# Performance work log

Measured on AMD Instinct MI355X. Metric: run time of the kernel, lower is better.

The kernel has to match this reference:

```python
import jax, jax.numpy as jnp
import numpy as np

N, D, H, E, OUT, TOP_K = 16384, 1024, 4096, 8, 4096, 2


def setup_inputs() -> dict:
    key = jax.random.key(0)
    ks = jax.random.split(key, 9)
    s_d = 1.0 / np.sqrt(D)
    s_h = 1.0 / np.sqrt(H)
    return {
        "x": jax.random.normal(ks[0], (N, D), dtype=jnp.float32),
        "W_in": jax.random.normal(ks[1], (D, D), dtype=jnp.float32) * s_d,
        "b_in": jax.random.normal(ks[2], (D,), dtype=jnp.float32) * 0.01,
        "W_gate": jax.random.normal(ks[3], (D, E), dtype=jnp.float32) * s_d,
        "W1": jax.random.normal(ks[4], (E, D, H), dtype=jnp.float32) * s_d,
        "b1": jax.random.normal(ks[5], (E, H), dtype=jnp.float32) * 0.01,
        "W2": jax.random.normal(ks[6], (E, H, D), dtype=jnp.float32) * s_h,
        "b2": jax.random.normal(ks[7], (E, D), dtype=jnp.float32) * 0.01,
        "W_head": jax.random.normal(ks[8], (D, OUT), dtype=jnp.float32) * s_d,
    }


def reference(x, W_in, b_in, W_gate, W1, b1, W2, b2, W_head):
    # Input linear: [N, D]
    h = x @ W_in + b_in

    # Gating: softmax over experts, keep top-k, renormalize
    probs = jax.nn.softmax(h @ W_gate, axis=-1)            # [N, E]
    top_vals, top_idx = jax.lax.top_k(probs, TOP_K)        # [N, K]
    top_vals = top_vals / jnp.sum(top_vals, axis=-1, keepdims=True)
    rows = jnp.arange(h.shape[0])[:, None]
    combine = jnp.zeros_like(probs).at[rows, top_idx].set(top_vals)  # [N, E]

    # Expert FFNs, weighted combine (loop over small fixed expert count)
    moe_out = jnp.zeros_like(h)
    for e in range(E):
        he = jax.nn.relu(h @ W1[e] + b1[e])                # [N, H]
        ye = he @ W2[e] + b2[e]                            # [N, D]
        moe_out = moe_out + combine[:, e:e + 1] * ye

    # Head (no bias)
    return moe_out @ W_head
```

## Files before the change

kernel.cpp:

```cpp
#include <hip/hip_runtime.h>
#include <math.h>

#define NN 16384
#define DD 1024
#define HH 4096
#define EE 8
#define OUTD 4096

typedef unsigned short u16;
typedef short v8s __attribute__((ext_vector_type(8)));
typedef float v4f __attribute__((ext_vector_type(4)));

__device__ __forceinline__ u16 f2bf(float f) {
    unsigned int u = __float_as_uint(f);
    u = (u + 0x7fffu + ((u >> 16) & 1u)) >> 16;
    return (u16)u;
}

__device__ __forceinline__ void cp16(const u16* g, u16* l) {
    __builtin_amdgcn_global_load_lds(
        (const __attribute__((address_space(1))) unsigned int*)g,
        (__attribute__((address_space(3))) unsigned int*)l, 16, 0, 0);
}

__global__ __launch_bounds__(256) void cvt_bf16(const float* __restrict__ in,
                                                u16* __restrict__ out, int n4) {
    int i = blockIdx.x * 256 + threadIdx.x;
    if (i < n4) {
        float4 v = ((const float4*)in)[i];
        ushort4 o;
        o.x = f2bf(v.x); o.y = f2bf(v.y); o.z = f2bf(v.z); o.w = f2bf(v.w);
        ((ushort4*)out)[i] = o;
    }
}

__global__ __launch_bounds__(256) void transpose_cast(const float* __restrict__ in,
                                                      u16* __restrict__ out,
                                                      int rows, int cols) {
    __shared__ float t[32][33];
    const float* inp = in + (size_t)blockIdx.z * rows * cols;
    u16* outp = out + (size_t)blockIdx.z * rows * cols;
    int c0 = blockIdx.x * 32, r0 = blockIdx.y * 32;
    int tx = threadIdx.x & 31, ty = threadIdx.x >> 5;
#pragma unroll
    for (int i = 0; i < 4; ++i)
        t[ty + i * 8][tx] = inp[(size_t)(r0 + ty + i * 8) * cols + c0 + tx];
    __syncthreads();
#pragma unroll
    for (int i = 0; i < 4; ++i)
        outp[(size_t)(c0 + ty + i * 8) * rows + r0 + tx] = f2bf(t[tx][ty + i * 8]);
}

__global__ __launch_bounds__(256) void compute_G(const float* __restrict__ Win,
                                                 const float* __restrict__ Wg,
                                                 const float* __restrict__ b_in,
                                                 float* __restrict__ Gt,
                                                 float* __restrict__ cvec) {
    int tid = blockIdx.x * 256 + threadIdx.x;
    if (tid < EE * DD) {
        int e = tid >> 10, d = tid & 1023;
        float s = 0.f;
        for (int j = 0; j < DD; ++j) s += Win[(size_t)d * DD + j] * Wg[j * EE + e];
        Gt[e * DD + d] = s;
    } else if (tid < EE * DD + EE) {
        int e = tid - EE * DD;
        float s = 0.f;
        for (int j = 0; j < DD; ++j) s += b_in[j] * Wg[j * EE + e];
        cvec[e] = s;
    }
}

__global__ __launch_bounds__(256) void gate_kernel(const float* __restrict__ x,
                                                   const float* __restrict__ Gt,
                                                   const float* __restrict__ cvec,
                                                   int* __restrict__ counts,
                                                   int* __restrict__ toklist,
                                                   float* __restrict__ wtlist) {
    int wave = threadIdx.x >> 6, lane = threadIdx.x & 63;
    int t = blockIdx.x * 4 + wave;
    const float* xr = x + (size_t)t * DD;
    float p[EE];
#pragma unroll
    for (int e = 0; e < EE; ++e) p[e] = 0.f;
    for (int it = 0; it < DD / 64; ++it) {
        int d = it * 64 + lane;
        float xv = xr[d];
#pragma unroll
        for (int e = 0; e < EE; ++e) p[e] += xv * Gt[e * DD + d];
    }
#pragma unroll
    for (int e = 0; e < EE; ++e) {
        float v = p[e];
#pragma unroll
        for (int m = 32; m >= 1; m >>= 1) v += __shfl_xor(v, m);
        p[e] = v;
    }
    if (lane == 0) {
        float l[EE];
#pragma unroll
        for (int e = 0; e < EE; ++e) l[e] = p[e] + cvec[e];
        int i0 = 0; float v0 = l[0];
#pragma unroll
        for (int e = 1; e < EE; ++e) if (l[e] > v0) { v0 = l[e]; i0 = e; }
        int i1 = -1; float v1 = -1e30f;
#pragma unroll
        for (int e = 0; e < EE; ++e) if (e != i0 && l[e] > v1) { v1 = l[e]; i1 = e; }
        float e1 = __expf(v1 - v0);
        float inv = 1.f / (1.f + e1);
        float w0 = inv, w1 = e1 * inv;
        int pos0 = atomicAdd(&counts[i0], 1);
        toklist[i0 * NN + pos0] = t; wtlist[i0 * NN + pos0] = w0;
        int pos1 = atomicAdd(&counts[i1], 1);
        toklist[i1 * NN + pos1] = t; wtlist[i1 * NN + pos1] = w1;
    }
}

__global__ void offsets_kernel(const int* __restrict__ counts, int* __restrict__ offs) {
    if (threadIdx.x == 0) {
        int a = 0;
        for (int e = 0; e < EE; ++e) { offs[e] = a; a += counts[e]; }
    }
}

template <int MODE, int K, int LDC>
__global__ __launch_bounds__(256, 2) void gemm_bt(
    const u16* __restrict__ A, const u16* __restrict__ Btb,
    u16* __restrict__ outb, float* __restrict__ outf,
    const float* __restrict__ biasb,
    const int* __restrict__ toklist, const float* __restrict__ wtlist,
    const int* __restrict__ counts, const int* __restrict__ offsets,
    float* __restrict__ moe) {
    __shared__ __align__(16) u16 As[128 * 32];
    __shared__ __align__(16) u16 Bs[128 * 32];

    int e = 0, mt = blockIdx.x, cnt = 0, ofs = 0;
    if (MODE == 1 || MODE == 2) {
        e = blockIdx.x >> 7; mt = blockIdx.x & 127;
        cnt = counts[e];
        if (mt * 128 >= cnt) return;
        ofs = offsets[e];
    }
    const int m0 = mt * 128;
    const int n0 = blockIdx.y * 128;

    const u16* Bt = Btb;
    const float* bias = biasb;
    if (MODE == 1) { Bt += (size_t)e * HH * DD; bias += e * HH; }
    if (MODE == 2) { Bt += (size_t)e * DD * HH; bias += e * DD; }

    const int lane = threadIdx.x & 63;
    const int wave = threadIdx.x >> 6;
    const int rl = lane >> 2;
    const int kc = lane & 3;

    const u16* aS[2];
    const u16* bS[2];
    u16* aL[2];
    u16* bL[2];
#pragma unroll
    for (int s = 0; s < 2; ++s) {
        int trow = wave * 32 + s * 16 + rl;
        long arow;
        if (MODE == 1) {
            int rr = m0 + trow; if (rr >= cnt) rr = cnt - 1;
            arow = toklist[e * NN + rr];
        } else if (MODE == 2) {
            int rr = m0 + trow; if (rr >= cnt) rr = cnt - 1;
            arow = ofs + rr;
        } else {
            arow = m0 + trow;
        }
        aS[s] = A + (size_t)arow * K + kc * 8;
        bS[s] = Bt + (size_t)(n0 + trow) * K + kc * 8;
        aL[s] = &As[(wave * 32 + s * 16) * 32];
        bL[s] = &Bs[(wave * 32 + s * 16) * 32];
    }

    const int wm = wave & 1, wn = wave >> 1;
    const int fr = lane & 15;
    const int kof = (lane >> 4) * 8;

    v4f acc[4][4];
#pragma unroll
    for (int i = 0; i < 4; ++i)
#pragma unroll
        for (int j = 0; j < 4; ++j)
#pragma unroll
            for (int c = 0; c < 4; ++c) acc[i][j][c] = 0.f;

    for (int k0 = 0; k0 < K; k0 += 32) {
        __syncthreads();
#pragma unroll
        for (int s = 0; s < 2; ++s) {
            cp16(aS[s] + k0, aL[s]);
            cp16(bS[s] + k0, bL[s]);
        }
        asm volatile("s_waitcnt vmcnt(0)" ::: "memory");
        __syncthreads();

        v8s af[4], bf[4];
#pragma unroll
        for (int i = 0; i < 4; ++i)
            af[i] = *(const v8s*)&As[(wm * 64 + i * 16 + fr) * 32 + kof];
#pragma unroll
        for (int j = 0; j < 4; ++j)
            bf[j] = *(const v8s*)&Bs[(wn * 64 + j * 16 + fr) * 32 + kof];
#pragma unroll
        for (int i = 0; i < 4; ++i)
#pragma unroll
            for (int j = 0; j < 4; ++j)
                acc[i][j] = __builtin_amdgcn_mfma_f32_16x16x32_bf16(af[i], bf[j], acc[i][j], 0, 0, 0);
    }

    const int quad = (lane >> 4) * 4;
#pragma unroll
    for (int i = 0; i < 4; ++i) {
#pragma unroll
        for (int r = 0; r < 4; ++r) {
            int rloc = wm * 64 + i * 16 + quad + r;
            int grow = m0 + rloc;
            if ((MODE == 1 || MODE == 2) && grow >= cnt) continue;
            int tok = 0; float wgt = 0.f;
            if (MODE == 2) { tok = toklist[e * NN + grow]; wgt = wtlist[e * NN + grow]; }
#pragma unroll
            for (int j = 0; j < 4; ++j) {
                int col = n0 + wn * 64 + j * 16 + fr;
                float v = acc[i][j][r];
                if (MODE == 0) {
                    outb[(size_t)grow * LDC + col] = f2bf(v + bias[col]);
                } else if (MODE == 1) {
                    float t = v + bias[col];
                    t = t > 0.f ? t : 0.f;
                    outb[(size_t)(ofs + grow) * LDC + col] = f2bf(t);
                } else if (MODE == 2) {
                    atomicAdd(&moe[(size_t)tok * LDC + col], wgt * (v + bias[col]));
                } else {
                    outf[(size_t)grow * LDC + col] = v;
                }
            }
        }
    }
}

extern "C" void kernel_launch(void* const* d_in, const int* in_sizes, int n_in,
                              void* d_out, int out_size, void* d_ws, size_t ws_size,
                              hipStream_t stream) {
    const float* x    = (const float*)d_in[0];
    const float* Win  = (const float*)d_in[1];
    const float* b_in = (const float*)d_in[2];
    const float* Wg   = (const float*)d_in[3];
    const float* W1   = (const float*)d_in[4];
    const float* b1   = (const float*)d_in[5];
    const float* W2   = (const float*)d_in[6];
    const float* b2   = (const float*)d_in[7];
    const float* Wh   = (const float*)d_in[8];
    float* out = (float*)d_out;

    char* p = (char*)d_ws;
    size_t off = 0;
    auto alloc = [&](size_t bytes) {
        char* r = p + off;
        off = (off + bytes + 255) & ~(size_t)255;
        return r;
    };
    u16*   x_bf   = (u16*)alloc((size_t)NN * DD * 2);
    u16*   wint   = (u16*)alloc((size_t)DD * DD * 2);
    u16*   w1t    = (u16*)alloc((size_t)EE * DD * HH * 2);
    u16*   w2t    = (u16*)alloc((size_t)EE * DD * HH * 2);
    u16*   wht    = (u16*)alloc((size_t)DD * OUTD * 2);
    u16*   h_bf   = (u16*)alloc((size_t)NN * DD * 2);
    float* moe_f  = (float*)alloc((size_t)NN * DD * 4);
    u16*   moe_bf = (u16*)alloc((size_t)NN * DD * 2);
    float* Gt     = (float*)alloc((size_t)EE * DD * 4);
    float* cvec   = (float*)alloc(256);
    int*   counts = (int*)alloc(256);
    int*   offs   = (int*)alloc(256);
    int*   tok    = (int*)alloc((size_t)EE * NN * 4);
    float* wt     = (float*)alloc((size_t)EE * NN * 4);
    if (off > ws_size) return;

    u16* he = (u16*)d_out;

    hipMemsetAsync(counts, 0, 256, stream);
    hipMemsetAsync(moe_f, 0, (size_t)NN * DD * 4, stream);

    cvt_bf16<<<dim3(NN * DD / 4 / 256), 256, 0, stream>>>(x, x_bf, NN * DD / 4);
    transpose_cast<<<dim3(DD / 32, DD / 32, 1), 256, 0, stream>>>(Win, wint, DD, DD);
    transpose_cast<<<dim3(HH / 32, DD / 32, EE), 256, 0, stream>>>(W1, w1t, DD, HH);
    transpose_cast<<<dim3(DD / 32, HH / 32, EE), 256, 0, stream>>>(W2, w2t, HH, DD);
    transpose_cast<<<dim3(OUTD / 32, DD / 32, 1), 256, 0, stream>>>(Wh, wht, DD, OUTD);
    compute_G<<<dim3((EE * DD + EE + 255) / 256), 256, 0, stream>>>(Win, Wg, b_in, Gt, cvec);

    gemm_bt<0, DD, DD><<<dim3(NN / 128, DD / 128), 256, 0, stream>>>(
        x_bf, wint, h_bf, nullptr, b_in, nullptr, nullptr, nullptr, nullptr, nullptr);

    gate_kernel<<<dim3(NN / 4), 256, 0, stream>>>(x, Gt, cvec, counts, tok, wt);
    offsets_kernel<<<dim3(1), 64, 0, stream>>>(counts, offs);

    gemm_bt<1, DD, HH><<<dim3(EE * 128, HH / 128), 256, 0, stream>>>(
        h_bf, w1t, he, nullptr, b1, tok, wt, counts, offs, nullptr);

    gemm_bt<2, HH, DD><<<dim3(EE * 128, DD / 128), 256, 0, stream>>>(
        he, w2t, nullptr, nullptr, b2, tok, wt, counts, offs, moe_f);

    cvt_bf16<<<dim3(NN * DD / 4 / 256), 256, 0, stream>>>(moe_f, moe_bf, NN * DD / 4);

    gemm_bt<3, DD, OUTD><<<dim3(NN / 128, OUTD / 128), 256, 0, stream>>>(
        moe_bf, wht, nullptr, out, nullptr, nullptr, nullptr, nullptr, nullptr, nullptr);
}
```

Baseline: 2.460 ms.

## Triple-buffer GEMM LDS loads with swizzled layout and XCD-aware block mapping

Turns the single-buffered K loop into a 3-stage pipeline. Async global-to-LDS copies for tile k+2 are issued while tile k is computed, with partial vmcnt waits in place of full drains. The LDS K-chunk index is XOR-swizzled to reduce bank conflicts on fragment reads. Workgroup IDs are remapped so neighbouring tiles land on the same XCD for L2 reuse, and MFMA sections get raised wave priority. Tripling LDS use (48KB per block) may limit occupancy at 2 blocks per CU, and the swizzle requires the grid size to be divisible by 8.

```diff
diff --git a/kernel.cpp b/kernel.cpp
--- a/kernel.cpp
+++ b/kernel.cpp
@@ -130,18 +130,29 @@
     const int* __restrict__ toklist, const float* __restrict__ wtlist,
     const int* __restrict__ counts, const int* __restrict__ offsets,
     float* __restrict__ moe) {
-    __shared__ __align__(16) u16 As[128 * 32];
-    __shared__ __align__(16) u16 Bs[128 * 32];
-
-    int e = 0, mt = blockIdx.x, cnt = 0, ofs = 0;
+    __shared__ __align__(16) u16 As[3][128 * 32];
+    __shared__ __align__(16) u16 Bs[3][128 * 32];
+
+    constexpr int GX = (MODE == 1 || MODE == 2) ? EE * 128 : NN / 128;
+    constexpr int GY = LDC / 128;
+    constexpr int NWG = GX * GY;
+    constexpr int QC = NWG / 8;
+    static_assert(NWG % 8 == 0, "xcd swizzle needs nwg%8==0");
+
+    const int wg = blockIdx.x + GX * blockIdx.y;
+    const int lid = (wg & 7) * QC + (wg >> 3);
+    const int bx = lid & (GX - 1);
+    const int by = lid / GX;
+
+    int e = 0, mt = bx, cnt = 0, ofs = 0;
     if (MODE == 1 || MODE == 2) {
-        e = blockIdx.x >> 7; mt = blockIdx.x & 127;
+        e = bx >> 7; mt = bx & 127;
         cnt = counts[e];
         if (mt * 128 >= cnt) return;
         ofs = offsets[e];
     }
     const int m0 = mt * 128;
-    const int n0 = blockIdx.y * 128;
+    const int n0 = by * 128;
 
     const u16* Bt = Btb;
     const float* bias = biasb;
@@ -152,11 +163,10 @@
     const int wave = threadIdx.x >> 6;
     const int rl = lane >> 2;
     const int kc = lane & 3;
+    const int kcs = kc ^ ((rl >> 1) & 3);
 
     const u16* aS[2];
     const u16* bS[2];
-    u16* aL[2];
-    u16* bL[2];
 #pragma unroll
     for (int s = 0; s < 2; ++s) {
         int trow = wave * 32 + s * 16 + rl;
@@ -170,15 +180,15 @@
         } else {
             arow = m0 + trow;
         }
-        aS[s] = A + (size_t)arow * K + kc * 8;
-        bS[s] = Bt + (size_t)(n0 + trow) * K + kc * 8;
-        aL[s] = &As[(wave * 32 + s * 16) * 32];
-        bL[s] = &Bs[(wave * 32 + s * 16) * 32];
-    }
+        aS[s] = A + (size_t)arow * K + kcs * 8;
+        bS[s] = Bt + (size_t)(n0 + trow) * K + kcs * 8;
+    }
+    u16* aL[2] = { &As[0][(wave * 32) * 32], &As[0][(wave * 32 + 16) * 32] };
+    u16* bL[2] = { &Bs[0][(wave * 32) * 32], &Bs[0][(wave * 32 + 16) * 32] };
 
     const int wm = wave & 1, wn = wave >> 1;
     const int fr = lane & 15;
-    const int kof = (lane >> 4) * 8;
+    const int kswz = ((lane >> 4) ^ ((fr >> 1) & 3)) * 8;
 
     v4f acc[4][4];
 #pragma unroll
@@ -188,28 +198,51 @@
 #pragma unroll
             for (int c = 0; c < 4; ++c) acc[i][j][c] = 0.f;
 
-    for (int k0 = 0; k0 < K; k0 += 32) {
-        __syncthreads();
+    auto STAGE = [&](int kt, int buf) {
 #pragma unroll
         for (int s = 0; s < 2; ++s) {
-            cp16(aS[s] + k0, aL[s]);
-            cp16(bS[s] + k0, bL[s]);
+            cp16(aS[s] + kt * 32, aL[s] + buf * 4096);
+            cp16(bS[s] + kt * 32, bL[s] + buf * 4096);
         }
-        asm volatile("s_waitcnt vmcnt(0)" ::: "memory");
-        __syncthreads();
-
-        v8s af[4], bf[4];
+    };
+
+    constexpr int NIT = K / 32;
+    STAGE(0, 0);
+    STAGE(1, 1);
+
+    int cur = 0, pre = 2;
+    for (int it = 0; it < NIT; ++it) {
+        if (it + 2 < NIT) {
+            STAGE(it + 2, pre);
+            asm volatile("s_waitcnt vmcnt(8)" ::: "memory");
+        } else if (it + 2 == NIT) {
+            asm volatile("s_waitcnt vmcnt(4)" ::: "memory");
+        } else {
+            asm volatile("s_waitcnt vmcnt(0)" ::: "memory");
+        }
+        __builtin_amdgcn_s_barrier();
+        asm volatile("" ::: "memory");
+
+        v8s af[4], bv[4];
 #pragma unroll
         for (int i = 0; i < 4; ++i)
-            af[i] = *(const v8s*)&As[(wm * 64 + i * 16 + fr) * 32 + kof];
+            af[i] = *(const v8s*)&As[cur][(wm * 64 + i * 16 + fr) * 32 + kswz];
 #pragma unroll
         for (int j = 0; j < 4; ++j)
-            bf[j] = *(const v8s*)&Bs[(wn * 64 + j * 16 + fr) * 32 + kof];
+            bv[j] = *(const v8s*)&Bs[cur][(wn * 64 + j * 16 + fr) * 32 + kswz];
+
+        __builtin_amdgcn_s_setprio(1);
 #pragma unroll
         for (int i = 0; i < 4; ++i)
 #pragma unroll
             for (int j = 0; j < 4; ++j)
-                acc[i][j] = __builtin_amdgcn_mfma_f32_16x16x32_bf16(af[i], bf[j], acc[i][j], 0, 0, 0);
+                acc[i][j] = __builtin_amdgcn_mfma_f32_16x16x32_bf16(af[i], bv[j], acc[i][j], 0, 0, 0);
+        __builtin_amdgcn_s_setprio(0);
+
+        asm volatile("" ::: "memory");
+        __builtin_amdgcn_s_barrier();
+        cur = cur == 2 ? 0 : cur + 1;
+        pre = pre == 2 ? 0 : pre + 1;
     }
 
     const int quad = (lane >> 4) * 4;
```

Result: faster. 2.170 ms (-11.8%).
